# Performance work log

Hardware: AMD Instinct MI355X
Metric: run time of the kernel (lower is better)

Reference implementation:

```python
import jax, jax.numpy as jnp
import numpy as np

S, V, L = 64, 16, 5            # hn_dim=(64,16), num_layers=5
ED, RD, TD = 16, 16, 64        # edge_dim, rbf_dim, t_dim
N, EL, EG, B = 16384, 131072, 262144, 64
FIN = 2 * S + RD + ED          # per-edge message input width
H = S + 2 * V                  # message output: scalar msg + 2 vector gates
CUT_L, CUT_G = 3.0, 10.0


def _ln(x, g, b, eps=1e-5):
    m = x.mean(-1, keepdims=True)
    var = ((x - m) ** 2).mean(-1, keepdims=True)
    return (x - m) / jnp.sqrt(var + eps) * g + b


def _seg_mean(x, idx, n):
    s = jax.ops.segment_sum(x, idx, num_segments=n)
    c = jax.ops.segment_sum(jnp.ones((x.shape[0], 1), x.dtype), idx, num_segments=n)
    return s / jnp.maximum(c, 1.0)


def _edge_geom(ei, pos, cutoff):
    src, tgt = ei[0], ei[1]
    r = pos[tgt] - pos[src]                       # [E,3]
    d = jnp.sqrt(jnp.clip((r * r).sum(-1), 1e-6))
    rn = r / d[:, None]
    centers = jnp.linspace(0.0, cutoff, RD)
    width = cutoff / RD
    env = jnp.where(d < cutoff, 0.5 * (jnp.cos(jnp.pi * d / cutoff) + 1.0), 0.0)
    rbf = jnp.exp(-0.5 * ((d[:, None] - centers) / width) ** 2) * env[:, None]
    return src, tgt, rn, rbf


def setup_inputs() -> dict:
    key = jax.random.key(0)
    ks = iter(jax.random.split(key, 32))
    nrm = lambda shp, sc=1.0: jax.random.normal(next(ks), shp, jnp.float32) * sc
    x = jax.random.randint(next(ks), (N, 3), 0, 16)
    t = nrm((B, TD))
    pos = nrm((N, 3))
    eil = jax.random.randint(next(ks), (2, EL), 0, N)
    eig = jax.random.randint(next(ks), (2, EG), 0, N)
    eal = jax.random.randint(next(ks), (EL,), 0, 5)
    eag = jax.random.randint(next(ks), (EG,), 0, 5)
    batch = jnp.sort(jax.random.randint(next(ks), (N,), 0, B))
    return dict(
        x=x, t=t, pos=pos,
        edge_index_local=eil, edge_index_global=eig,
        edge_attr_local=eal, edge_attr_global=eag, batch=batch,
        atom_emb=nrm((3, 16, S), 0.1),
        bond_emb=nrm((5, ED), 0.1),
        t_w1=nrm((TD, TD), TD ** -0.5), t_b1=jnp.zeros(TD),
        t_w2=nrm((TD, S), TD ** -0.5), t_b2=jnp.zeros(S),
        gnn_wm=nrm((L, 2, FIN, H), FIN ** -0.5), gnn_bm=jnp.zeros((L, 2, H)),
        gnn_wu=nrm((L, 2, S, S), S ** -0.5), gnn_bu=jnp.zeros((L, 2, S)),
        ln_g=jnp.ones((L, S)), ln_b=jnp.zeros((L, S)),
        head_dscore_w=nrm((S, 1), S ** -0.5),
        head_out_w=nrm((V, 1), V ** -0.5),
    )


def reference(x, t, pos, edge_index_local, edge_index_global, edge_attr_local,
              edge_attr_global, batch, atom_emb, bond_emb, t_w1, t_b1, t_w2,
              t_b2, gnn_wm, gnn_bm, gnn_wu, gnn_bu, ln_g, ln_b,
              head_dscore_w, head_out_w):
    n = x.shape[0]
    # AtomEncoder: sum of per-feature-column embeddings; + broadcast t-embedding
    s = atom_emb[0][x[:, 0]] + atom_emb[1][x[:, 1]] + atom_emb[2][x[:, 2]]
    temb = jax.nn.silu(jax.nn.silu(t @ t_w1 + t_b1) @ t_w2 + t_b2)
    s = s + temb[batch]
    v = jnp.zeros((n, 3, V), s.dtype)

    edge_sets = []
    for ei, ea, cut in ((edge_index_local, edge_attr_local, CUT_L),
                        (edge_index_global, edge_attr_global, CUT_G)):
        src, tgt, rn, rbf = _edge_geom(ei, pos, cut)
        edge_sets.append((src, tgt, rn, rbf, bond_emb[ea]))

    for i in range(L):
        for k, (src, tgt, rn, rbf, e) in enumerate(edge_sets):
            feat = jnp.concatenate([s[src], s[tgt], rbf, e], -1)       # [E,FIN]
            h = jax.nn.silu(feat @ gnn_wm[i, k] + gnn_bm[i, k])        # [E,H]
            ms, wv1, wv2 = h[:, :S], h[:, S:S + V], h[:, S + V:]
            vm = v[src] * wv1[:, None, :] + rn[:, :, None] * wv2[:, None, :]
            agg_s = _seg_mean(ms, tgt, n)                              # [N,S]
            agg_v = _seg_mean(vm.reshape(-1, 3 * V), tgt, n).reshape(n, 3, V)
            s = s + jax.nn.silu(agg_s @ gnn_wu[i, k] + gnn_bu[i, k])
            v = v + agg_v
        s = _ln(s, ln_g[i], ln_b[i])

    # ScoreHead (conservative=False)
    dsc = jax.nn.silu(s) @ head_dscore_w                               # [N,1]
    src, tgt = edge_index_global[0], edge_index_global[1]
    sr = (dsc[src] + dsc[tgt]) * (pos[src] - pos[tgt])                 # [E,3]
    sr = jax.ops.segment_sum(sr, tgt, num_segments=n)                  # [N,3]
    score = (v @ head_out_w)[..., 0] + sr                              # [N,3]
    return score
```

## Files before the change

kernel.cpp:

```cpp
#include <hip/hip_runtime.h>
#include <math.h>

#define Sdim 64
#define Vdim 16
#define NLAYER 5
#define EDdim 16
#define RDdim 16
#define TDdim 64
#define FINdim 160
#define Hdim 96
#define NVdim 48

typedef __attribute__((ext_vector_type(8))) short bf16x8;
typedef __attribute__((ext_vector_type(4))) float f32x4;

__device__ __forceinline__ float silu_f(float x) {
    return x / (1.0f + __expf(-x));
}

__device__ __forceinline__ unsigned short f2bf(float x) {
    union { float f; unsigned u; } v; v.f = x;
    unsigned r = v.u + 0x7fffu + ((v.u >> 16) & 1u);
    return (unsigned short)(r >> 16);
}

__device__ __forceinline__ float bf2f(unsigned short u) {
    union { unsigned u; float f; } v; v.u = (unsigned)u << 16;
    return v.f;
}

__global__ __launch_bounds__(256) void pack_kernel(
    const float* __restrict__ wm, const float* __restrict__ bemb,
    unsigned short* __restrict__ wp, unsigned short* __restrict__ bondbf)
{
    int idx = blockIdx.x * 256 + threadIdx.x;
    if (idx < 10 * FINdim * Hdim) {
        int ls = idx / (FINdim * Hdim), rem = idx % (FINdim * Hdim);
        int k = rem / Hdim, c = rem % Hdim;
        wp[(size_t)ls * FINdim * Hdim + ((size_t)(k >> 3) * Hdim + c) * 8 + (k & 7)] =
            f2bf(wm[idx]);
    } else if (idx < 10 * FINdim * Hdim + 80) {
        int i = idx - 10 * FINdim * Hdim;
        bondbf[i] = f2bf(bemb[i]);
    }
}

__global__ __launch_bounds__(64) void temb_kernel(
    const float* __restrict__ t, const float* __restrict__ w1, const float* __restrict__ b1,
    const float* __restrict__ w2, const float* __restrict__ b2, float* __restrict__ temb)
{
    int b = blockIdx.x, j = threadIdx.x;
    __shared__ float row[TDdim];
    __shared__ float hid[TDdim];
    row[j] = t[b * TDdim + j];
    __syncthreads();
    float h = b1[j];
    #pragma unroll 8
    for (int i = 0; i < TDdim; ++i) h = fmaf(row[i], w1[i * TDdim + j], h);
    h = silu_f(h);
    hid[j] = h;
    __syncthreads();
    float o = b2[j];
    #pragma unroll 8
    for (int i = 0; i < TDdim; ++i) o = fmaf(hid[i], w2[i * Sdim + j], o);
    temb[b * Sdim + j] = silu_f(o);
}

__global__ __launch_bounds__(256) void node_init_kernel(
    const int* __restrict__ x, const int* __restrict__ batch,
    const float* __restrict__ aemb, const float* __restrict__ temb,
    float* __restrict__ sfeat, unsigned short* __restrict__ sbf, int n)
{
    int idx = blockIdx.x * 256 + threadIdx.x;
    if (idx >= n * Sdim) return;
    int node = idx >> 6, j = idx & 63;
    int x0 = x[node * 3 + 0], x1 = x[node * 3 + 1], x2 = x[node * 3 + 2];
    float v = aemb[(0 * 16 + x0) * Sdim + j] + aemb[(16 + x1) * Sdim + j]
            + aemb[(32 + x2) * Sdim + j] + temb[batch[node] * Sdim + j];
    sfeat[idx] = v;
    sbf[idx]   = f2bf(v);
}

__global__ __launch_bounds__(256) void count_kernel(
    const int* __restrict__ ei, int E, int* __restrict__ counts)
{
    int e = blockIdx.x * 256 + threadIdx.x;
    if (e >= E) return;
    atomicAdd(&counts[ei[E + e]], 1);
}

__global__ __launch_bounds__(256) void scan_kernel(
    const int* __restrict__ counts, int n,
    int* __restrict__ rowStart, int* __restrict__ cursor)
{
    __shared__ int wsum[4];
    int t = threadIdx.x;
    int chunk = n / 256;
    int base = t * chunk;
    int s = 0;
    for (int i = 0; i < chunk; ++i) s += counts[base + i];
    int lane = t & 63, w = t >> 6;
    int sc = s;
    #pragma unroll
    for (int off = 1; off < 64; off <<= 1) {
        int xv = __shfl_up(sc, off);
        if (lane >= off) sc += xv;
    }
    if (lane == 63) wsum[w] = sc;
    __syncthreads();
    int woff = 0;
    for (int i = 0; i < w; ++i) woff += wsum[i];
    int off = woff + sc - s;
    for (int i = 0; i < chunk; ++i) {
        rowStart[base + i] = off;
        cursor[base + i]   = off;
        off += counts[base + i];
    }
    if (t == 255) rowStart[n] = off;
}

__global__ __launch_bounds__(256) void scatter_kernel(
    const int* __restrict__ ei, const int* __restrict__ ea, int E,
    int* __restrict__ cursor, int2* __restrict__ st2, int* __restrict__ eaS)
{
    int e = blockIdx.x * 256 + threadIdx.x;
    if (e >= E) return;
    int tgt = ei[E + e];
    int p = atomicAdd(&cursor[tgt], 1);
    st2[p] = make_int2(ei[e], tgt);
    eaS[p] = ea[e];
}

__global__ __launch_bounds__(256) void geom_kernel(
    const float* __restrict__ pos,
    const int2* __restrict__ st2, const int* __restrict__ eaS,
    const unsigned short* __restrict__ bondbf,
    float4* __restrict__ rn4, unsigned short* __restrict__ rbfb,
    int E, float cutoff)
{
    int e = blockIdx.x * 256 + threadIdx.x;
    if (e >= E) return;
    int2 st = st2[e];
    int s = st.x, t = st.y;
    float rx = pos[3*t]-pos[3*s], ry = pos[3*t+1]-pos[3*s+1], rz = pos[3*t+2]-pos[3*s+2];
    float d = sqrtf(fmaxf(rx*rx + ry*ry + rz*rz, 1e-6f));
    float invd = 1.0f / d;
    rn4[e] = make_float4(rx*invd, ry*invd, rz*invd, d);
    float env = (d < cutoff) ? 0.5f * (__cosf(3.14159265358979f * d / cutoff) + 1.0f) : 0.0f;
    float invw = (float)RDdim / cutoff;
    unsigned int pk[8];
    #pragma unroll
    for (int i2 = 0; i2 < 8; ++i2) {
        float c0 = cutoff * ((float)(2*i2)     / 15.0f);
        float c1 = cutoff * ((float)(2*i2 + 1) / 15.0f);
        float t0 = (d - c0) * invw, t1 = (d - c1) * invw;
        unsigned short b0 = f2bf(__expf(-0.5f * t0 * t0) * env);
        unsigned short b1 = f2bf(__expf(-0.5f * t1 * t1) * env);
        pk[i2] = (unsigned)b0 | ((unsigned)b1 << 16);
    }
    uint4* o = reinterpret_cast<uint4*>(rbfb + (size_t)e * 32);
    o[0] = make_uint4(pk[0], pk[1], pk[2], pk[3]);
    o[1] = make_uint4(pk[4], pk[5], pk[6], pk[7]);
    int ea = eaS[e];
    const uint4* bp = reinterpret_cast<const uint4*>(bondbf + ea * EDdim);
    o[2] = bp[0];
    o[3] = bp[1];
}

__global__ __launch_bounds__(256) void edge_mlp_kernel(
    const unsigned short* __restrict__ sbf_in,
    const int2* __restrict__ st2,
    const unsigned short* __restrict__ rbfb,
    const unsigned short* __restrict__ wpk,
    const float* __restrict__ bg,
    unsigned short* __restrict__ hm,
    unsigned short* __restrict__ hv)
{
    __shared__ __align__(16) unsigned short Wl[FINdim * Hdim];
    {
        const uint4* s4 = reinterpret_cast<const uint4*>(wpk);
        uint4* d4 = reinterpret_cast<uint4*>(Wl);
        for (int i = threadIdx.x; i < FINdim * Hdim / 8; i += 256) d4[i] = s4[i];
    }
    __syncthreads();

    const int lane = threadIdx.x & 63;
    const int wid  = threadIdx.x >> 6;
    const int l15 = lane & 15, l4 = lane >> 4;
    const int base0 = blockIdx.x * 128 + wid * 16;
    const int base1 = base0 + 64;

    const int2 st0 = st2[base0 + l15];
    const int2 st1 = st2[base1 + l15];
    bf16x8 a0[5], a1[5];
    {
        const unsigned short* sp = sbf_in + (size_t)st0.x * Sdim;
        const unsigned short* tp = sbf_in + (size_t)st0.y * Sdim;
        a0[0] = *reinterpret_cast<const bf16x8*>(sp + l4 * 8);
        a0[1] = *reinterpret_cast<const bf16x8*>(sp + 32 + l4 * 8);
        a0[2] = *reinterpret_cast<const bf16x8*>(tp + l4 * 8);
        a0[3] = *reinterpret_cast<const bf16x8*>(tp + 32 + l4 * 8);
        a0[4] = *reinterpret_cast<const bf16x8*>(rbfb + (size_t)(base0 + l15) * 32 + l4 * 8);
    }
    {
        const unsigned short* sp = sbf_in + (size_t)st1.x * Sdim;
        const unsigned short* tp = sbf_in + (size_t)st1.y * Sdim;
        a1[0] = *reinterpret_cast<const bf16x8*>(sp + l4 * 8);
        a1[1] = *reinterpret_cast<const bf16x8*>(sp + 32 + l4 * 8);
        a1[2] = *reinterpret_cast<const bf16x8*>(tp + l4 * 8);
        a1[3] = *reinterpret_cast<const bf16x8*>(tp + 32 + l4 * 8);
        a1[4] = *reinterpret_cast<const bf16x8*>(rbfb + (size_t)(base1 + l15) * 32 + l4 * 8);
    }

    f32x4 acc0[6], acc1[6];
    #pragma unroll
    for (int nt = 0; nt < 6; ++nt) {
        acc0[nt] = (f32x4){0.f, 0.f, 0.f, 0.f};
        acc1[nt] = (f32x4){0.f, 0.f, 0.f, 0.f};
    }
    #pragma unroll
    for (int kk = 0; kk < 5; ++kk) {
        #pragma unroll
        for (int nt = 0; nt < 6; ++nt) {
            bf16x8 b = *reinterpret_cast<const bf16x8*>(
                Wl + ((size_t)(kk * 4 + l4) * Hdim + nt * 16 + l15) * 8);
            acc0[nt] = __builtin_amdgcn_mfma_f32_16x16x32_bf16(a0[kk], b, acc0[nt], 0, 0, 0);
            acc1[nt] = __builtin_amdgcn_mfma_f32_16x16x32_bf16(a1[kk], b, acc1[nt], 0, 0, 0);
        }
    }

    #pragma unroll
    for (int nt = 0; nt < 6; ++nt) {
        const float bs = bg[nt * 16 + l15];
        #pragma unroll
        for (int r = 0; r < 4; ++r) {
            const int e0 = base0 + l4 * 4 + r;
            const int e1 = base1 + l4 * 4 + r;
            const unsigned short h0 = f2bf(silu_f(acc0[nt][r] + bs));
            const unsigned short h1 = f2bf(silu_f(acc1[nt][r] + bs));
            if (nt < 4) {
                hm[(size_t)e0 * 64 + nt * 16 + l15] = h0;
                hm[(size_t)e1 * 64 + nt * 16 + l15] = h1;
            } else {
                hv[(size_t)e0 * 32 + (nt - 4) * 16 + l15] = h0;
                hv[(size_t)e1 * 32 + (nt - 4) * 16 + l15] = h1;
            }
        }
    }
}

__global__ __launch_bounds__(64) void node_agg_kernel(
    const float* __restrict__ s_in, float* __restrict__ s_out,
    unsigned short* __restrict__ sbf_out,
    const float* __restrict__ v_in, float* __restrict__ v_out,
    const int* __restrict__ rowStart, const int2* __restrict__ st2,
    const float* __restrict__ rn4f,
    const unsigned short* __restrict__ hm, const unsigned short* __restrict__ hv,
    const float* __restrict__ wu, const float* __restrict__ bu,
    const float* __restrict__ lng, const float* __restrict__ lnb,
    int do_ln)
{
    const int node = blockIdx.x;
    const int lane = threadIdx.x;
    const int l15 = lane & 15, dd = lane >> 4;
    const int lo = rowStart[node], hi = rowStart[node + 1];

    float msum = 0.0f, vsum = 0.0f;
    for (int e = lo; e < hi; ++e) {
        msum += bf2f(hm[(size_t)e * 64 + lane]);
        if (lane < NVdim) {
            float wv1 = bf2f(hv[(size_t)e * 32 + l15]);
            float wv2 = bf2f(hv[(size_t)e * 32 + 16 + l15]);
            float rnd = rn4f[(size_t)e * 4 + dd];
            int srcN  = st2[e].x;
            float vv  = v_in[(size_t)srcN * NVdim + lane];
            vsum = fmaf(vv, wv1, fmaf(rnd, wv2, vsum));
        }
    }

    __shared__ float ag[64];
    const float ic = 1.0f / fmaxf((float)(hi - lo), 1.0f);
    ag[lane] = msum * ic;

    float dot = 0.0f;
    #pragma unroll 8
    for (int i = 0; i < Sdim; ++i) dot = fmaf(ag[i], wu[i * Sdim + lane], dot);
    float sn = s_in[(size_t)node * Sdim + lane] + silu_f(dot + bu[lane]);
    if (do_ln) {
        float mm = sn;
        #pragma unroll
        for (int off = 32; off >= 1; off >>= 1) mm += __shfl_xor(mm, off);
        mm *= (1.0f / 64.0f);
        float dv = sn - mm;
        float var = dv * dv;
        #pragma unroll
        for (int off = 32; off >= 1; off >>= 1) var += __shfl_xor(var, off);
        var *= (1.0f / 64.0f);
        sn = dv * rsqrtf(var + 1e-5f) * lng[lane] + lnb[lane];
    }
    s_out[(size_t)node * Sdim + lane]   = sn;
    sbf_out[(size_t)node * Sdim + lane] = f2bf(sn);
    if (lane < NVdim)
        v_out[(size_t)node * NVdim + lane] =
            v_in[(size_t)node * NVdim + lane] + vsum * ic;
}

__global__ __launch_bounds__(64) void head1_kernel(
    const float* __restrict__ sfeat, const float* __restrict__ vfeat,
    const float* __restrict__ wd, const float* __restrict__ wo,
    float* __restrict__ dsc, float* __restrict__ out)
{
    int node = blockIdx.x, j = threadIdx.x;
    float val = silu_f(sfeat[(size_t)node * Sdim + j]) * wd[j];
    #pragma unroll
    for (int off = 32; off >= 1; off >>= 1) val += __shfl_xor(val, off);
    if (j == 0) dsc[node] = val;
    if (j < 3) {
        float a = 0.0f;
        #pragma unroll
        for (int m = 0; m < Vdim; ++m)
            a += vfeat[(size_t)node * NVdim + j * Vdim + m] * wo[m];
        out[(size_t)node * 3 + j] = a;
    }
}

__global__ __launch_bounds__(256) void head2_kernel(
    const float* __restrict__ dsc, const int* __restrict__ rsG,
    const int2* __restrict__ st2G, const float4* __restrict__ rn4G,
    float* __restrict__ out, int n)
{
    int t = blockIdx.x * 256 + threadIdx.x;
    if (t >= n) return;
    int lo = rsG[t], hi = rsG[t + 1];
    float dt = dsc[t];
    float ax = 0.f, ay = 0.f, az = 0.f;
    for (int e = lo; e < hi; ++e) {
        float w = dsc[st2G[e].x] + dt;
        float4 rn = rn4G[e];
        float wd_ = w * rn.w;
        ax -= wd_ * rn.x; ay -= wd_ * rn.y; az -= wd_ * rn.z;
    }
    out[3 * t + 0] += ax;
    out[3 * t + 1] += ay;
    out[3 * t + 2] += az;
}

extern "C" void kernel_launch(void* const* d_in, const int* in_sizes, int n_in,
                              void* d_out, int out_size, void* d_ws, size_t ws_size,
                              hipStream_t stream)
{
    const int*   x     = (const int*)d_in[0];
    const float* t     = (const float*)d_in[1];
    const float* pos   = (const float*)d_in[2];
    const int*   eil   = (const int*)d_in[3];
    const int*   eig   = (const int*)d_in[4];
    const int*   eal   = (const int*)d_in[5];
    const int*   eag   = (const int*)d_in[6];
    const int*   batch = (const int*)d_in[7];
    const float* aemb  = (const float*)d_in[8];
    const float* bemb  = (const float*)d_in[9];
    const float* t_w1  = (const float*)d_in[10];
    const float* t_b1  = (const float*)d_in[11];
    const float* t_w2  = (const float*)d_in[12];
    const float* t_b2  = (const float*)d_in[13];
    const float* wm    = (const float*)d_in[14];
    const float* bm    = (const float*)d_in[15];
    const float* wu    = (const float*)d_in[16];
    const float* bu    = (const float*)d_in[17];
    const float* lng   = (const float*)d_in[18];
    const float* lnb   = (const float*)d_in[19];
    const float* wd    = (const float*)d_in[20];
    const float* wo    = (const float*)d_in[21];

    const int n  = in_sizes[7];
    const int B  = in_sizes[1] / TDdim;
    const int EL = in_sizes[3] / 2;
    const int EG = in_sizes[4] / 2;

    char* p = (char*)d_ws;
    auto alignup = [](char* q) { return (char*)(((size_t)q + 15) & ~(size_t)15); };

    float* temb = (float*)p;                 p += (size_t)B * Sdim * 4;
    float* dsc  = (float*)p;                 p += (size_t)n * 4;
    float* sA   = (float*)p;                 p += (size_t)n * Sdim * 4;
    float* sB   = (float*)p;                 p += (size_t)n * Sdim * 4;
    float* vA   = (float*)p;                 p += (size_t)n * NVdim * 4;
    float* vB   = (float*)p;                 p += (size_t)n * NVdim * 4;
    int* counts = (int*)p;                   p += (size_t)n * 4;
    int* cursor = (int*)p;                   p += (size_t)n * 4;
    int* rsL    = (int*)p;                   p += (size_t)(n + 4) * 4;
    int* rsG    = (int*)p;                   p += (size_t)(n + 4) * 4;
    int* eaL2   = (int*)p;                   p += (size_t)EL * 4;
    int* eaG2   = (int*)p;                   p += (size_t)EG * 4;
    p = alignup(p);
    int2* st2L  = (int2*)p;                  p += (size_t)EL * 8;
    int2* st2G  = (int2*)p;                  p += (size_t)EG * 8;
    p = alignup(p);
    unsigned short* wp     = (unsigned short*)p;  p += (size_t)10 * FINdim * Hdim * 2;
    p = alignup(p);
    unsigned short* bondbf = (unsigned short*)p;  p += 96 * 2;
    p = alignup(p);
    unsigned short* sbfA   = (unsigned short*)p;  p += (size_t)n * Sdim * 2;
    unsigned short* sbfB   = (unsigned short*)p;  p += (size_t)n * Sdim * 2;
    p = alignup(p);
    float4* rn4L = (float4*)p;               p += (size_t)EL * 16;
    float4* rn4G = (float4*)p;               p += (size_t)EG * 16;
    unsigned short* rbfbL = (unsigned short*)p;  p += (size_t)EL * 32 * 2;
    unsigned short* rbfbG = (unsigned short*)p;  p += (size_t)EG * 32 * 2;
    p = alignup(p);
    unsigned short* hm = (unsigned short*)p; p += (size_t)EG * 64 * 2;
    unsigned short* hv = (unsigned short*)p; p += (size_t)EG * 32 * 2;

    float* out = (float*)d_out;

    pack_kernel<<<(10 * FINdim * Hdim + 80 + 255) / 256, 256, 0, stream>>>(wm, bemb, wp, bondbf);
    temb_kernel<<<B, 64, 0, stream>>>(t, t_w1, t_b1, t_w2, t_b2, temb);
    node_init_kernel<<<(n * Sdim + 255) / 256, 256, 0, stream>>>(x, batch, aemb, temb, sA, sbfA, n);
    hipMemsetAsync(vA, 0, (size_t)n * NVdim * sizeof(float), stream);

    hipMemsetAsync(counts, 0, (size_t)n * sizeof(int), stream);
    count_kernel<<<(EL + 255) / 256, 256, 0, stream>>>(eil, EL, counts);
    scan_kernel<<<1, 256, 0, stream>>>(counts, n, rsL, cursor);
    scatter_kernel<<<(EL + 255) / 256, 256, 0, stream>>>(eil, eal, EL, cursor, st2L, eaL2);

    hipMemsetAsync(counts, 0, (size_t)n * sizeof(int), stream);
    count_kernel<<<(EG + 255) / 256, 256, 0, stream>>>(eig, EG, counts);
    scan_kernel<<<1, 256, 0, stream>>>(counts, n, rsG, cursor);
    scatter_kernel<<<(EG + 255) / 256, 256, 0, stream>>>(eig, eag, EG, cursor, st2G, eaG2);

    geom_kernel<<<(EL + 255) / 256, 256, 0, stream>>>(pos, st2L, eaL2, bondbf, rn4L, rbfbL, EL, 3.0f);
    geom_kernel<<<(EG + 255) / 256, 256, 0, stream>>>(pos, st2G, eaG2, bondbf, rn4G, rbfbG, EG, 10.0f);

    float* s_cur = sA; float* s_nxt = sB;
    float* v_cur = vA; float* v_nxt = vB;
    unsigned short* sb_cur = sbfA; unsigned short* sb_nxt = sbfB;

    for (int l = 0; l < NLAYER; ++l) {
        for (int k = 0; k < 2; ++k) {
            int ls = l * 2 + k;
            const unsigned short* wpk = wp + (size_t)ls * FINdim * Hdim;
            const float* bgk = bm + (size_t)ls * Hdim;
            const float* wuk = wu + (size_t)ls * Sdim * Sdim;
            const float* buk = bu + (size_t)ls * Sdim;
            const int E          = (k == 0) ? EL : EG;
            const int2* st2k     = (k == 0) ? st2L : st2G;
            const int* rsk       = (k == 0) ? rsL : rsG;
            const float4* rn4k   = (k == 0) ? rn4L : rn4G;
            const unsigned short* rbfbk = (k == 0) ? rbfbL : rbfbG;

            edge_mlp_kernel<<<E / 128, 256, 0, stream>>>(
                sb_cur, st2k, rbfbk, wpk, bgk, hm, hv);
            node_agg_kernel<<<n, 64, 0, stream>>>(
                s_cur, s_nxt, sb_nxt, v_cur, v_nxt,
                rsk, st2k, (const float*)rn4k, hm, hv,
                wuk, buk, lng + (size_t)l * Sdim, lnb + (size_t)l * Sdim,
                (k == 1) ? 1 : 0);

            float* tmp = s_cur; s_cur = s_nxt; s_nxt = tmp;
            tmp = v_cur; v_cur = v_nxt; v_nxt = tmp;
            unsigned short* tb = sb_cur; sb_cur = sb_nxt; sb_nxt = tb;
        }
    }

    head1_kernel<<<n, 64, 0, stream>>>(s_cur, v_cur, wd, wo, dsc, out);
    head2_kernel<<<(n + 255) / 256, 256, 0, stream>>>(dsc, rsG, st2G, rn4G, out, n);
}
```

Baseline: 686.0 us.

## Merge local and global CSR build and geometry into combined preprocessing kernels

```diff
diff --git a/kernel.cpp b/kernel.cpp
--- a/kernel.cpp
+++ b/kernel.cpp
@@ -81,21 +81,27 @@
     sbf[idx]   = f2bf(v);
 }
 
-__global__ __launch_bounds__(256) void count_kernel(
-    const int* __restrict__ ei, int E, int* __restrict__ counts)
-{
-    int e = blockIdx.x * 256 + threadIdx.x;
-    if (e >= E) return;
-    atomicAdd(&counts[ei[E + e]], 1);
+__global__ __launch_bounds__(256) void count_all_kernel(
+    const int* __restrict__ eil, int EL,
+    const int* __restrict__ eig, int EG,
+    int* __restrict__ counts, int n)
+{
+    int idx = blockIdx.x * 256 + threadIdx.x;
+    if (idx < EL) {
+        atomicAdd(&counts[eil[EL + idx]], 1);
+    } else if (idx < EL + EG) {
+        int j = idx - EL;
+        atomicAdd(&counts[n + eig[EG + j]], 1);
+    }
 }
 
 __global__ __launch_bounds__(256) void scan_kernel(
-    const int* __restrict__ counts, int n,
+    const int* __restrict__ counts, int n2,
     int* __restrict__ rowStart, int* __restrict__ cursor)
 {
     __shared__ int wsum[4];
     int t = threadIdx.x;
-    int chunk = n / 256;
+    int chunk = n2 / 256;
     int base = t * chunk;
     int s = 0;
     for (int i = 0; i < chunk; ++i) s += counts[base + i];
@@ -116,36 +122,36 @@
         cursor[base + i]   = off;
         off += counts[base + i];
     }
-    if (t == 255) rowStart[n] = off;
-}
-
-__global__ __launch_bounds__(256) void scatter_kernel(
-    const int* __restrict__ ei, const int* __restrict__ ea, int E,
-    int* __restrict__ cursor, int2* __restrict__ st2, int* __restrict__ eaS)
-{
-    int e = blockIdx.x * 256 + threadIdx.x;
-    if (e >= E) return;
-    int tgt = ei[E + e];
-    int p = atomicAdd(&cursor[tgt], 1);
-    st2[p] = make_int2(ei[e], tgt);
-    eaS[p] = ea[e];
-}
-
-__global__ __launch_bounds__(256) void geom_kernel(
-    const float* __restrict__ pos,
-    const int2* __restrict__ st2, const int* __restrict__ eaS,
-    const unsigned short* __restrict__ bondbf,
-    float4* __restrict__ rn4, unsigned short* __restrict__ rbfb,
-    int E, float cutoff)
-{
-    int e = blockIdx.x * 256 + threadIdx.x;
-    if (e >= E) return;
-    int2 st = st2[e];
-    int s = st.x, t = st.y;
-    float rx = pos[3*t]-pos[3*s], ry = pos[3*t+1]-pos[3*s+1], rz = pos[3*t+2]-pos[3*s+2];
+    if (t == 255) rowStart[n2] = off;
+}
+
+__global__ __launch_bounds__(256) void scatgeom_kernel(
+    const int* __restrict__ eil, const int* __restrict__ eal, int EL,
+    const int* __restrict__ eig, const int* __restrict__ eag, int EG,
+    int* __restrict__ cursor, int n,
+    const float* __restrict__ pos, const unsigned short* __restrict__ bondbf,
+    int2* __restrict__ st2, float4* __restrict__ rn4,
+    unsigned short* __restrict__ rbfb)
+{
+    int idx = blockIdx.x * 256 + threadIdx.x;
+    if (idx >= EL + EG) return;
+    int src, tgt, ea, cbase;
+    float cutoff;
+    if (idx < EL) {
+        src = eil[idx]; tgt = eil[EL + idx]; ea = eal[idx];
+        cbase = 0; cutoff = 3.0f;
+    } else {
+        int j = idx - EL;
+        src = eig[j]; tgt = eig[EG + j]; ea = eag[j];
+        cbase = n; cutoff = 10.0f;
+    }
+    int p = atomicAdd(&cursor[cbase + tgt], 1);
+    st2[p] = make_int2(src, tgt);
+
+    float rx = pos[3*tgt]-pos[3*src], ry = pos[3*tgt+1]-pos[3*src+1], rz = pos[3*tgt+2]-pos[3*src+2];
     float d = sqrtf(fmaxf(rx*rx + ry*ry + rz*rz, 1e-6f));
     float invd = 1.0f / d;
-    rn4[e] = make_float4(rx*invd, ry*invd, rz*invd, d);
+    rn4[p] = make_float4(rx*invd, ry*invd, rz*invd, d);
     float env = (d < cutoff) ? 0.5f * (__cosf(3.14159265358979f * d / cutoff) + 1.0f) : 0.0f;
     float invw = (float)RDdim / cutoff;
     unsigned int pk[8];
@@ -158,10 +164,9 @@
         unsigned short b1 = f2bf(__expf(-0.5f * t1 * t1) * env);
         pk[i2] = (unsigned)b0 | ((unsigned)b1 << 16);
     }
-    uint4* o = reinterpret_cast<uint4*>(rbfb + (size_t)e * 32);
+    uint4* o = reinterpret_cast<uint4*>(rbfb + (size_t)p * 32);
     o[0] = make_uint4(pk[0], pk[1], pk[2], pk[3]);
     o[1] = make_uint4(pk[4], pk[5], pk[6], pk[7]);
-    int ea = eaS[e];
     const uint4* bp = reinterpret_cast<const uint4*>(bondbf + ea * EDdim);
     o[2] = bp[0];
     o[3] = bp[1];
@@ -174,7 +179,8 @@
     const unsigned short* __restrict__ wpk,
     const float* __restrict__ bg,
     unsigned short* __restrict__ hm,
-    unsigned short* __restrict__ hv)
+    unsigned short* __restrict__ hv,
+    int eOff)
 {
     __shared__ __align__(16) unsigned short Wl[FINdim * Hdim];
     {
@@ -187,7 +193,7 @@
     const int lane = threadIdx.x & 63;
     const int wid  = threadIdx.x >> 6;
     const int l15 = lane & 15, l4 = lane >> 4;
-    const int base0 = blockIdx.x * 128 + wid * 16;
+    const int base0 = eOff + blockIdx.x * 128 + wid * 16;
     const int base1 = base0 + 64;
 
     const int2 st0 = st2[base0 + l15];
@@ -258,25 +264,50 @@
     const unsigned short* __restrict__ hm, const unsigned short* __restrict__ hv,
     const float* __restrict__ wu, const float* __restrict__ bu,
     const float* __restrict__ lng, const float* __restrict__ lnb,
-    int do_ln)
+    int do_ln, int v_zero)
 {
     const int node = blockIdx.x;
     const int lane = threadIdx.x;
     const int l15 = lane & 15, dd = lane >> 4;
     const int lo = rowStart[node], hi = rowStart[node + 1];
 
-    float msum = 0.0f, vsum = 0.0f;
-    for (int e = lo; e < hi; ++e) {
-        msum += bf2f(hm[(size_t)e * 64 + lane]);
+    float msum0 = 0.0f, msum1 = 0.0f, vsum0 = 0.0f, vsum1 = 0.0f;
+    int e = lo;
+    for (; e + 1 < hi; e += 2) {
+        msum0 += bf2f(hm[(size_t)e * 64 + lane]);
+        msum1 += bf2f(hm[(size_t)(e + 1) * 64 + lane]);
+        if (lane < NVdim) {
+            float wv1a = bf2f(hv[(size_t)e * 32 + l15]);
+            float wv2a = bf2f(hv[(size_t)e * 32 + 16 + l15]);
+            float rnda = rn4f[(size_t)e * 4 + dd];
+            float wv1b = bf2f(hv[(size_t)(e + 1) * 32 + l15]);
+            float wv2b = bf2f(hv[(size_t)(e + 1) * 32 + 16 + l15]);
+            float rndb = rn4f[(size_t)(e + 1) * 4 + dd];
+            vsum0 = fmaf(rnda, wv2a, vsum0);
+            vsum1 = fmaf(rndb, wv2b, vsum1);
+            if (!v_zero) {
+                float vva = v_in[(size_t)st2[e].x * NVdim + lane];
+                float vvb = v_in[(size_t)st2[e + 1].x * NVdim + lane];
+                vsum0 = fmaf(vva, wv1a, vsum0);
+                vsum1 = fmaf(vvb, wv1b, vsum1);
+            }
+        }
+    }
+    if (e < hi) {
+        msum0 += bf2f(hm[(size_t)e * 64 + lane]);
         if (lane < NVdim) {
             float wv1 = bf2f(hv[(size_t)e * 32 + l15]);
             float wv2 = bf2f(hv[(size_t)e * 32 + 16 + l15]);
             float rnd = rn4f[(size_t)e * 4 + dd];
-            int srcN  = st2[e].x;
-            float vv  = v_in[(size_t)srcN * NVdim + lane];
-            vsum = fmaf(vv, wv1, fmaf(rnd, wv2, vsum));
+            vsum0 = fmaf(rnd, wv2, vsum0);
+            if (!v_zero) {
+                float vv = v_in[(size_t)st2[e].x * NVdim + lane];
+                vsum0 = fmaf(vv, wv1, vsum0);
+            }
         }
     }
+    float msum = msum0 + msum1;
+    float vsum = vsum0 + vsum1;
 
     __shared__ float ag[64];
     const float ic = 1.0f / fmaxf((float)(hi - lo), 1.0f);
@@ -300,9 +331,10 @@
     }
     s_out[(size_t)node * Sdim + lane]   = sn;
     sbf_out[(size_t)node * Sdim + lane] = f2bf(sn);
-    if (lane < NVdim)
-        v_out[(size_t)node * NVdim + lane] =
-            v_in[(size_t)node * NVdim + lane] + vsum * ic;
+    if (lane < NVdim) {
+        float vprev = v_zero ? 0.0f : v_in[(size_t)node * NVdim + lane];
+        v_out[(size_t)node * NVdim + lane] = vprev + vsum * ic;
+    }
 }
 
 __global__ __launch_bounds__(64) void head1_kernel(
@@ -326,7 +358,7 @@
 
 __global__ __launch_bounds__(256) void head2_kernel(
     const float* __restrict__ dsc, const int* __restrict__ rsG,
-    const int2* __restrict__ st2G, const float4* __restrict__ rn4G,
+    const int2* __restrict__ st2, const float4* __restrict__ rn4,
     float* __restrict__ out, int n)
 {
     int t = blockIdx.x * 256 + threadIdx.x;
@@ -335,8 +367,8 @@
     float dt = dsc[t];
     float ax = 0.f, ay = 0.f, az = 0.f;
     for (int e = lo; e < hi; ++e) {
-        float w = dsc[st2G[e].x] + dt;
-        float4 rn = rn4G[e];
+        float w = dsc[st2[e].x] + dt;
+        float4 rn = rn4[e];
         float wd_ = w * rn.w;
         ax -= wd_ * rn.x; ay -= wd_ * rn.y; az -= wd_ * rn.z;
     }
@@ -376,6 +408,7 @@
     const int B  = in_sizes[1] / TDdim;
     const int EL = in_sizes[3] / 2;
     const int EG = in_sizes[4] / 2;
+    const int ET = EL + EG;
 
     char* p = (char*)d_ws;
     auto alignup = [](char* q) { return (char*)(((size_t)q + 15) & ~(size_t)15); };
@@ -386,15 +419,11 @@
     float* sB   = (float*)p;                 p += (size_t)n * Sdim * 4;
     float* vA   = (float*)p;                 p += (size_t)n * NVdim * 4;
     float* vB   = (float*)p;                 p += (size_t)n * NVdim * 4;
-    int* counts = (int*)p;                   p += (size_t)n * 4;
-    int* cursor = (int*)p;                   p += (size_t)n * 4;
-    int* rsL    = (int*)p;                   p += (size_t)(n + 4) * 4;
-    int* rsG    = (int*)p;                   p += (size_t)(n + 4) * 4;
-    int* eaL2   = (int*)p;                   p += (size_t)EL * 4;
-    int* eaG2   = (int*)p;                   p += (size_t)EG * 4;
-    p = alignup(p);
-    int2* st2L  = (int2*)p;                  p += (size_t)EL * 8;
-    int2* st2G  = (int2*)p;                  p += (size_t)EG * 8;
+    int* counts = (int*)p;                   p += (size_t)(2 * n) * 4;
+    int* cursor = (int*)p;                   p += (size_t)(2 * n) * 4;
+    int* rsAll  = (int*)p;                   p += (size_t)(2 * n + 4) * 4;
+    p = alignup(p);
+    int2* st2   = (int2*)p;                  p += (size_t)ET * 8;
     p = alignup(p);
     unsigned short* wp     = (unsigned short*)p;  p += (size_t)10 * FINdim * Hdim * 2;
     p = alignup(p);
@@ -403,33 +432,23 @@
     unsigned short* sbfA   = (unsigned short*)p;  p += (size_t)n * Sdim * 2;
     unsigned short* sbfB   = (unsigned short*)p;  p += (size_t)n * Sdim * 2;
     p = alignup(p);
-    float4* rn4L = (float4*)p;               p += (size_t)EL * 16;
-    float4* rn4G = (float4*)p;               p += (size_t)EG * 16;
-    unsigned short* rbfbL = (unsigned short*)p;  p += (size_t)EL * 32 * 2;
-    unsigned short* rbfbG = (unsigned short*)p;  p += (size_t)EG * 32 * 2;
-    p = alignup(p);
-    unsigned short* hm = (unsigned short*)p; p += (size_t)EG * 64 * 2;
-    unsigned short* hv = (unsigned short*)p; p += (size_t)EG * 32 * 2;
+    float4* rn4 = (float4*)p;                p += (size_t)ET * 16;
+    unsigned short* rbfb = (unsigned short*)p;    p += (size_t)ET * 32 * 2;
+    p = alignup(p);
+    unsigned short* hm = (unsigned short*)p; p += (size_t)ET * 64 * 2;
+    unsigned short* hv = (unsigned short*)p; p += (size_t)ET * 32 * 2;
 
     float* out = (float*)d_out;
 
     pack_kernel<<<(10 * FINdim * Hdim + 80 + 255) / 256, 256, 0, stream>>>(wm, bemb, wp, bondbf);
     temb_kernel<<<B, 64, 0, stream>>>(t, t_w1, t_b1, t_w2, t_b2, temb);
     node_init_kernel<<<(n * Sdim + 255) / 256, 256, 0, stream>>>(x, batch, aemb, temb, sA, sbfA, n);
-    hipMemsetAsync(vA, 0, (size_t)n * NVdim * sizeof(float), stream);
-
-    hipMemsetAsync(counts, 0, (size_t)n * sizeof(int), stream);
-    count_kernel<<<(EL + 255) / 256, 256, 0, stream>>>(eil, EL, counts);
-    scan_kernel<<<1, 256, 0, stream>>>(counts, n, rsL, cursor);
-    scatter_kernel<<<(EL + 255) / 256, 256, 0, stream>>>(eil, eal, EL, cursor, st2L, eaL2);
-
-    hipMemsetAsync(counts, 0, (size_t)n * sizeof(int), stream);
-    count_kernel<<<(EG + 255) / 256, 256, 0, stream>>>(eig, EG, counts);
-    scan_kernel<<<1, 256, 0, stream>>>(counts, n, rsG, cursor);
-    scatter_kernel<<<(EG + 255) / 256, 256, 0, stream>>>(eig, eag, EG, cursor, st2G, eaG2);
-
-    geom_kernel<<<(EL + 255) / 256, 256, 0, stream>>>(pos, st2L, eaL2, bondbf, rn4L, rbfbL, EL, 3.0f);
-    geom_kernel<<<(EG + 255) / 256, 256, 0, stream>>>(pos, st2G, eaG2, bondbf, rn4G, rbfbG, EG, 10.0f);
+
+    hipMemsetAsync(counts, 0, (size_t)(2 * n) * sizeof(int), stream);
+    count_all_kernel<<<(ET + 255) / 256, 256, 0, stream>>>(eil, EL, eig, EG, counts, n);
+    scan_kernel<<<1, 256, 0, stream>>>(counts, 2 * n, rsAll, cursor);
+    scatgeom_kernel<<<(ET + 255) / 256, 256, 0, stream>>>(
+        eil, eal, EL, eig, eag, EG, cursor, n, pos, bondbf, st2, rn4, rbfb);
 
     float* s_cur = sA; float* s_nxt = sB;
     float* v_cur = vA; float* v_nxt = vB;
@@ -442,19 +461,18 @@
             const float* bgk = bm + (size_t)ls * Hdim;
             const float* wuk = wu + (size_t)ls * Sdim * Sdim;
             const float* buk = bu + (size_t)ls * Sdim;
-            const int E          = (k == 0) ? EL : EG;
-            const int2* st2k     = (k == 0) ? st2L : st2G;
-            const int* rsk       = (k == 0) ? rsL : rsG;
-            const float4* rn4k   = (k == 0) ? rn4L : rn4G;
-            const unsigned short* rbfbk = (k == 0) ? rbfbL : rbfbG;
+            const int E    = (k == 0) ? EL : EG;
+            const int eOff = (k == 0) ? 0 : EL;
+            const int* rsk = (k == 0) ? rsAll : rsAll + n;
+            const int v_zero = (l == 0 && k == 0) ? 1 : 0;
 
             edge_mlp_kernel<<<E / 128, 256, 0, stream>>>(
-                sb_cur, st2k, rbfbk, wpk, bgk, hm, hv);
+                sb_cur, st2, rbfb, wpk, bgk, hm, hv, eOff);
             node_agg_kernel<<<n, 64, 0, stream>>>(
                 s_cur, s_nxt, sb_nxt, v_cur, v_nxt,
-                rsk, st2k, (const float*)rn4k, hm, hv,
+                rsk, st2, (const float*)rn4, hm, hv,
                 wuk, buk, lng + (size_t)l * Sdim, lnb + (size_t)l * Sdim,
-                (k == 1) ? 1 : 0);
+                (k == 1) ? 1 : 0, v_zero);
 
             float* tmp = s_cur; s_cur = s_nxt; s_nxt = tmp;
             tmp = v_cur; v_cur = v_nxt; v_nxt = tmp;
@@ -463,5 +481,5 @@
     }
 
     head1_kernel<<<n, 64, 0, stream>>>(s_cur, v_cur, wd, wo, dsc, out);
-    head2_kernel<<<(n + 255) / 256, 256, 0, stream>>>(dsc, rsG, st2G, rn4G, out, n);
-}
+    head2_kernel<<<(n + 255) / 256, 256, 0, stream>>>(dsc, rsAll + n, st2, rn4, out, n);
+}
```

Result: faster. 670.6 us (-2.2%).
